# Kernel optimization log

Measured on AMD Instinct MI355X. Metric: run time of the kernel, lower is better.

## Reference

```python
import jax, jax.numpy as jnp
import numpy as np

B, S, D, H = 2, 4096, 128, 128
EPS = 1e-6
NEG_INF = -1e30


def _complex_linear(xr, xi, Wr, Wi, br, bi):
    # x: (B,S,D); W: (H,D); complex linear (Wr + i Wi)(xr + i xi) + (br + i bi) per layer math:
    # real_out = (xr Wr + br) - (xi Wi + bi); imag_out = (xi Wr + br) + (xr Wi + bi)
    out_r = xr @ Wr.T + br - (xi @ Wi.T + bi)
    out_i = xi @ Wr.T + br + (xr @ Wi.T + bi)
    return out_r, out_i


def setup_inputs() -> dict:
    key = jax.random.key(0)
    ks = jax.random.split(key, 24)
    scale = 1.0 / np.sqrt(D)
    def W(k):
        return jax.random.normal(k, (H, D), jnp.float32) * scale
    def b(k):
        return jax.random.normal(k, (H,), jnp.float32) * 0.01
    inp = {
        "Z_q": jax.random.normal(ks[0], (B, 2, S, D, 1), jnp.float32),
        "Z_k": jax.random.normal(ks[1], (B, 2, S, D, 1), jnp.float32),
        "Z_v": jax.random.normal(ks[2], (B, 2, S, D, 1), jnp.float32),
        "Wq_r": W(ks[3]), "Wq_i": W(ks[4]), "bq_r": b(ks[5]), "bq_i": b(ks[6]),
        "Wk_r": W(ks[7]), "Wk_i": W(ks[8]), "bk_r": b(ks[9]), "bk_i": b(ks[10]),
        "Wv_r": W(ks[11]), "Wv_i": W(ks[12]), "bv_r": b(ks[13]), "bv_i": b(ks[14]),
        "Wp_r": W(ks[15]), "Wp_i": W(ks[16]), "bp_r": b(ks[17]), "bp_i": b(ks[18]),
        "noise_floor": jnp.asarray(1.0, jnp.float32),
        "tau": jnp.asarray(0.0, jnp.float32),
    }
    return inp


def reference(Z_q, Z_k, Z_v,
              Wq_r, Wq_i, bq_r, bq_i,
              Wk_r, Wk_i, bk_r, bk_i,
              Wv_r, Wv_i, bv_r, bv_i,
              Wp_r, Wp_i, bp_r, bp_i,
              noise_floor, tau):
    # squeeze trailing singleton; split real/imag -> (B,S,D)
    zqr, zqi = Z_q[:, 0, :, :, 0], Z_q[:, 1, :, :, 0]
    zkr, zki = Z_k[:, 0, :, :, 0], Z_k[:, 1, :, :, 0]
    zvr, zvi = Z_v[:, 0, :, :, 0], Z_v[:, 1, :, :, 0]

    Qr, Qi = _complex_linear(zqr, zqi, Wq_r, Wq_i, bq_r, bq_i)
    Kr, Ki = _complex_linear(zkr, zki, Wk_r, Wk_i, bk_r, bk_i)
    Vr, Vi = _complex_linear(zvr, zvi, Wv_r, Wv_i, bv_r, bv_i)

    # InverseMahalanobis: R2[b,i,j] = sum_h |Q[b,i]-K[b,j]|^2
    q2 = jnp.sum(Qr * Qr + Qi * Qi, axis=-1)          # (B,S)
    k2 = jnp.sum(Kr * Kr + Ki * Ki, axis=-1)          # (B,S)
    re_qk = (jnp.einsum('bsh,bth->bst', Qr, Kr)
             + jnp.einsum('bsh,bth->bst', Qi, Ki))    # (B,S,S)
    R2 = q2[:, :, None] + k2[:, None, :] - 2.0 * re_qk

    attn_scores = -jax.nn.softplus(tau) * jnp.log(noise_floor ** 2 + R2 + EPS)
    mask = jnp.tril(jnp.ones((S, S), dtype=bool))[None]
    attn_scores = jnp.where(mask, attn_scores, NEG_INF)
    attn_weights = jax.nn.softmax(attn_scores / jnp.sqrt(jnp.float32(H)), axis=-1)

    # attn (real) times complex V
    est_r = jnp.einsum('bst,bth->bsh', attn_weights, Vr)
    est_i = jnp.einsum('bst,bth->bsh', attn_weights, Vi)

    out_r, out_i = _complex_linear(est_r, est_i, Wp_r, Wp_i, bp_r, bp_i)
    out = jnp.stack((out_r, out_i), axis=1)[..., None]  # (B,2,S,H,1)
    return out, attn_weights
```

## Files before the change

kernel.cpp:

```cpp
#include <hip/hip_runtime.h>

#define S_LEN 4096
#define NBATCH 2
#define OUT_ELEMS 2097152

typedef _Float16 f16;
typedef _Float16 f16x8 __attribute__((ext_vector_type(8)));
typedef _Float16 f16x4 __attribute__((ext_vector_type(4)));
typedef float f32x4 __attribute__((ext_vector_type(4)));

#define MT_OFF    0x000000
#define BIAS_OFF  0x080000
#define SC_OFF    0x081000
#define QH_OFF    0x100000
#define KH_OFF    0x500000
#define VH_OFF    0x900000
#define Q2_OFF    0xD00000
#define K2_OFF    0xD10000
#define L_OFF     0xD20000
#define VPT_OFF   0xE00000
#define PW_OFF    0x1600000
#define WS_NEED   0x5600000

#define MFMA16(A,B,C) __builtin_amdgcn_mfma_f32_16x16x32_f16(A,B,C,0,0,0)

__device__ __forceinline__ void async_cp16(f16* lds, const f16* g) {
  __builtin_amdgcn_global_load_lds(
      (const __attribute__((address_space(1))) void*)g,
      (__attribute__((address_space(3))) void*)lds, 16, 0, 0);
}


__device__ __forceinline__ void stage16(f16* lds, const f16* g, int stride, int tid) {
#pragma unroll
  for (int i = 0; i < 2; ++i) {
    int idx = i*256 + tid;
    int row = idx >> 2, c = idx & 3;
    int cs = c ^ ((row >> 1) & 3);
    async_cp16(lds + idx*8, g + (size_t)row*stride + cs*8);
  }
}

__device__ __forceinline__ void stage32(f16* lds, const float* g, int stride, int tid) {
#pragma unroll
  for (int i = 0; i < 4; ++i) {
    int idx = i*256 + tid;
    int row = idx >> 3, c = idx & 7;
    const float4* gp = (const float4*)(g + (size_t)row*stride + c*4);
    float4 v = *gp;
    f16x4 h; h[0]=(f16)v.x; h[1]=(f16)v.y; h[2]=(f16)v.z; h[3]=(f16)v.w;
    int cl = (((c >> 1) ^ ((row >> 1) & 3)) << 1) | (c & 1);
    *(f16x4*)(lds + row*32 + cl*4) = h;
  }
}

__device__ __forceinline__ void mfma_step(const f16* Asm, const f16* Bsm, int lane,
                                          int wm, int wn, f32x4 acc[4][4]) {
  f16x8 a[4], b[4];
  int rr = lane & 15;
  int sc = (lane >> 4) ^ ((rr >> 1) & 3);
#pragma unroll
  for (int i=0;i<4;i++) a[i] = *(const f16x8*)(Asm + (wm + i*16 + rr)*32 + (sc<<3));
#pragma unroll
  for (int j=0;j<4;j++) b[j] = *(const f16x8*)(Bsm + (wn + j*16 + rr)*32 + (sc<<3));
#pragma unroll
  for (int i=0;i<4;i++)
#pragma unroll
    for (int j=0;j<4;j++) acc[i][j] = MFMA16(a[i], b[j], acc[i][j]);
}

__global__ __launch_bounds__(256)
void k_build(const float* Wqr, const float* Wqi, const float* bqr, const float* bqi,
             const float* Wkr, const float* Wki, const float* bkr, const float* bki,
             const float* Wvr, const float* Wvi, const float* bvr, const float* bvi,
             const float* Wpr, const float* Wpi, const float* bpr, const float* bpi,
             f16* Mt, float* bias) {
  int mat = blockIdx.x;
  const float *Wr, *Wi, *br, *bi;
  if (mat == 0)      { Wr=Wqr; Wi=Wqi; br=bqr; bi=bqi; }
  else if (mat == 1) { Wr=Wkr; Wi=Wki; br=bkr; bi=bki; }
  else if (mat == 2) { Wr=Wvr; Wi=Wvi; br=bvr; bi=bvi; }
  else               { Wr=Wpr; Wi=Wpi; br=bpr; bi=bpi; }
  int idx = blockIdx.y*256 + threadIdx.x;
  int n = idx >> 8, k = idx & 255;
  int d = k & 127, h = n & 127;
  float w = (k < 128) ? ((n < 128) ? Wr[h*128+d] : Wi[h*128+d])
                      : ((n < 128) ? -Wi[h*128+d] : Wr[h*128+d]);
  Mt[mat*65536 + n*256 + k] = (f16)w;
  if (k == 0)
    bias[mat*256 + n] = (n < 128) ? (br[n] - bi[n]) : (br[n-128] + bi[n-128]);
}

__global__ __launch_bounds__(256)
void k_init(float* outp, float* attn, float* zreg, float* sc, const float* bias,
            const float* nf, const float* tau) {
  int bx = blockIdx.x, tid = threadIdx.x;
  float4 z = make_float4(0.f,0.f,0.f,0.f);
  if (bx < 992) {
    int b = bx >= 496; int r = bx - b*496;
    int tb = 1; while (r >= tb) { r -= tb; tb++; }
    int sb = r;
    float* base = attn + ((size_t)(b*S_LEN) + sb*128)*S_LEN + tb*128;
    int c4 = tid & 31;
#pragma unroll
    for (int it = 0; it < 16; ++it) {
      int row = it*8 + (tid >> 5);
      *(float4*)(base + (size_t)row*S_LEN + c4*4) = z;
    }
    return;
  }
  int idx = (bx - 992)*256 + tid;
  if (idx < 524288) {
    int h4 = idx & 31;
    int comp = (idx >> 17) & 1;
    ((float4*)outp)[idx] = *(const float4*)(bias + 3*256 + comp*128 + h4*4);
  } else {
    int j = idx - 524288;
    if (j < 12288) ((float4*)zreg)[j] = z;
  }
  if (idx == 0) {
    float t = tau[0];
    float c = __builtin_log2f(1.0f + __builtin_exp2f(t * 1.4426950408889634f))
              * 0.6931471805599453f;
    sc[0] = -c * 0.08838834764831845f;
    sc[1] = nf[0]*nf[0] + 1e-6f;
  }
}

__global__ __launch_bounds__(256)
void k_proj(const float* Zq, const float* Zk, const float* Zv,
            const f16* Mt, const float* bias,
            f16* Qh, f16* Kh, f16* Vh, float* q2, float* k2) {
  __shared__ f16 Asm[2][128*32];
  __shared__ f16 Bsm[2][128*32];
  __shared__ float bias_s[128];
  int tid = threadIdx.x;
  int mode = blockIdx.z;
  int m0 = blockIdx.x * 128, n0 = blockIdx.y * 128;
  const float* Z = (mode==0) ? Zq : (mode==1 ? Zk : Zv);
  const f16* Bt = Mt + mode*65536;
  if (tid < 128) bias_s[tid] = bias[mode*256 + n0 + tid];
  int b = m0 >> 12, s0 = m0 & 4095;
  int lane = tid & 63, w = tid >> 6;
  int wm = (w >> 1)*64, wn = (w & 1)*64;
  f32x4 acc[4][4] = {};
  {
    const float* Ag = Z + (((size_t)(b*2 + 0))*S_LEN + s0)*128 + 0;
    stage32(Asm[0], Ag, 128, tid);
    stage16(Bsm[0], Bt + n0*256 + 0, 256, tid);
  }
  __syncthreads();
  for (int kb = 0; kb < 8; ++kb) {
    int cur = kb & 1;
    if (kb < 7) {
      int k1 = (kb+1)*32;
      int part = k1 >> 7, d0 = k1 & 127;
      const float* Ag = Z + (((size_t)(b*2 + part))*S_LEN + s0)*128 + d0;
      stage32(Asm[cur^1], Ag, 128, tid);
      stage16(Bsm[cur^1], Bt + n0*256 + k1, 256, tid);
    }
    mfma_step(Asm[cur], Bsm[cur], lane, wm, wn, acc);
    __syncthreads();
  }
  int rr = (lane>>4)*4, cc = lane & 15;
  f16* O = (mode==0) ? Qh : (mode==1 ? Kh : Vh);
  float rs[4][4];
#pragma unroll
  for (int i=0;i<4;i++)
#pragma unroll
    for (int r=0;r<4;r++) rs[i][r]=0.f;
#pragma unroll
  for (int i=0;i<4;i++)
#pragma unroll
    for (int j=0;j<4;j++) {
      int cl = wn + j*16 + cc;
      int cg = n0 + cl;
      float bv = bias_s[cl];
#pragma unroll
      for (int r=0;r<4;r++) {
        int rg = m0 + wm + i*16 + rr + r;
        f16 hv = (f16)(acc[i][j][r] + bv);
        O[(size_t)rg*256 + cg] = hv;
        float fv = (float)hv;
        rs[i][r] += fv*fv;
      }
    }
  if (mode < 2) {
#pragma unroll
    for (int m=8;m>=1;m>>=1)
#pragma unroll
      for (int i=0;i<4;i++)
#pragma unroll
        for (int r=0;r<4;r++) rs[i][r] += __shfl_xor(rs[i][r], m, 64);
    if (cc == 0) {
      float* T = (mode==0) ? q2 : k2;
#pragma unroll
      for (int i=0;i<4;i++)
#pragma unroll
        for (int r=0;r<4;r++) {
          int rg = m0 + wm + i*16 + rr + r;
          atomicAdd(&T[rg], rs[i][r]);
        }
    }
  }
}

__global__ __launch_bounds__(256)
void k_vp(const f16* Vh, const f16* Mt, f16* VPt) {
  __shared__ f16 Asm[2][128*32];
  __shared__ f16 Bsm[2][128*32];
  int t0 = blockIdx.x*128, n0 = blockIdx.y*128, b = blockIdx.z;
  int tid = threadIdx.x;
  int lane = tid & 63, w = tid >> 6;
  int wm = (w>>1)*64, wn = (w&1)*64;
  const f16* Ag = Mt + 3*65536 + n0*256;
  const f16* Bg = Vh + ((size_t)(b*S_LEN) + t0)*256;
  f32x4 acc[4][4] = {};
  stage16(Asm[0], Ag, 256, tid);
  stage16(Bsm[0], Bg, 256, tid);
  __syncthreads();
  for (int kb=0;kb<8;kb++) {
    int cur = kb & 1;
    if (kb < 7) {
      stage16(Asm[cur^1], Ag + (kb+1)*32, 256, tid);
      stage16(Bsm[cur^1], Bg + (kb+1)*32, 256, tid);
    }
    mfma_step(Asm[cur], Bsm[cur], lane, wm, wn, acc);
    __syncthreads();
  }
  int rr = (lane>>4)*4, cc = lane & 15;
#pragma unroll
  for (int i=0;i<4;i++) {
    int n = n0 + wm + i*16 + rr;
#pragma unroll
    for (int j=0;j<4;j++) {
      int t = t0 + wn + j*16 + cc;
#pragma unroll
      for (int r=0;r<4;r++)
        VPt[(size_t)b*1048576 + (size_t)(n + r)*4096 + t] = (f16)acc[i][j][r];
    }
  }
}

__global__ __launch_bounds__(256)
void k_attn(const f16* Qh, const f16* Kh, const float* q2, const float* k2,
            const float* sc, float* lsum, f16* Pws) {
  __shared__ f16 smem[4*128*32];
  __shared__ float q2s[128], k2s[128];
  f16* Asm0 = smem;
  f16* Asm1 = smem + 4096;
  f16* Bsm0 = smem + 8192;
  f16* Bsm1 = smem + 12288;
  int x = blockIdx.x;
  int b = x >= 528; int r = x - b*528;
  int sb = 0; while (r > sb) { r -= sb + 1; sb++; }
  int tb = r;
  int s0 = sb*128, t0 = tb*128;
  int tid = threadIdx.x;
  if (tid < 128) {
    q2s[tid] = q2[b*S_LEN + s0 + tid];
    k2s[tid] = k2[b*S_LEN + t0 + tid];
  }
  float kc = sc[0], nf2 = sc[1];
  int lane = tid & 63, w = tid >> 6;
  int wm = (w >> 1)*64, wn = (w & 1)*64;
  const f16* Ag = Qh + ((size_t)(b*S_LEN) + s0)*256;
  const f16* Bg = Kh + ((size_t)(b*S_LEN) + t0)*256;
  f32x4 acc[4][4] = {};
  stage16(Asm0, Ag, 256, tid);
  stage16(Bsm0, Bg, 256, tid);
  __syncthreads();
  for (int kb=0;kb<8;kb++) {
    int cur = kb & 1;
    if (kb < 7) {
      stage16(cur ? Asm0 : Asm1, Ag + (kb+1)*32, 256, tid);
      stage16(cur ? Bsm0 : Bsm1, Bg + (kb+1)*32, 256, tid);
    }
    mfma_step(cur ? Asm1 : Asm0, cur ? Bsm1 : Bsm0, lane, wm, wn, acc);
    __syncthreads();
  }
  f16* Psm = smem;
  int rr = (lane>>4)*4, cc = lane & 15;
  bool diag = (tb == sb);
  float rs[4][4];
#pragma unroll
  for (int i=0;i<4;i++)
#pragma unroll
    for (int rg=0;rg<4;rg++) rs[i][rg]=0.f;
#pragma unroll
  for (int i=0;i<4;i++)
#pragma unroll
    for (int j=0;j<4;j++) {
      int cl = wn + j*16 + cc;
      float kv = k2s[cl];
#pragma unroll
      for (int rg=0;rg<4;rg++) {
        int rl = wm + i*16 + rr + rg;
        float xx = nf2 + q2s[rl] + kv - 2.0f*acc[i][j][rg];
        float P = __builtin_exp2f(kc * __builtin_log2f(__builtin_fmaxf(xx, 1e-6f)));
        if (diag && (t0+cl) > (s0+rl)) P = 0.f;
        Psm[rl*128 + cl] = (f16)P;
        rs[i][rg] += P;
      }
    }
  __syncthreads();
  f16* Pg = Pws + ((size_t)(b*S_LEN) + s0)*S_LEN + t0;
#pragma unroll
  for (int i2 = 0; i2 < 8; ++i2) {
    int idx = i2*256 + tid;
    int row = idx >> 4, c = idx & 15;
    *(f16x8*)(Pg + (size_t)row*S_LEN + c*8) = *(const f16x8*)(Psm + row*128 + c*8);
  }
#pragma unroll
  for (int m=8;m>=1;m>>=1)
#pragma unroll
    for (int i=0;i<4;i++)
#pragma unroll
      for (int rg=0;rg<4;rg++) rs[i][rg] += __shfl_xor(rs[i][rg], m, 64);
  if (cc == 0)
#pragma unroll
    for (int i=0;i<4;i++)
#pragma unroll
      for (int rg=0;rg<4;rg++) {
        int rl = wm + i*16 + rr + rg;
        atomicAdd(&lsum[b*S_LEN + s0 + rl], rs[i][rg]);
      }
}

__global__ __launch_bounds__(256)
void k_pv(const f16* Pws, const f16* VPt, const float* lsum, float* outp, float* attn) {
  __shared__ f16 Asm[2][128*32];
  __shared__ f16 Bsm[2][128*32];
  __shared__ float ls[128];
  int r = blockIdx.x;
  int nb = blockIdx.y, b = blockIdx.z;
  int sb = 0;
  while (r >= ((sb+4)>>2)) { r -= (sb+4)>>2; sb++; }
  int c = r;
  int s0 = sb*128, h0 = nb*128;
  int tid = threadIdx.x;
  bool wrb = (nb == 0);
  if (tid < 128) ls[tid] = 1.0f / lsum[b*S_LEN + s0 + tid];
  int lane = tid & 63, w = tid >> 6;
  int wm = (w>>1)*64, wn = (w&1)*64;
  int tb0 = c*4, tb1 = tb0 + 4; if (tb1 > sb+1) tb1 = sb+1;
  int nt = (tb1 - tb0) * 4;
  int base_t = tb0*128;
  const f16* Abase = Pws + ((size_t)(b*S_LEN) + s0)*S_LEN + base_t;
  const f16* Bbase = VPt + (size_t)b*1048576 + (size_t)h0*4096 + base_t;
  f32x4 acc[4][4] = {};
  int row2 = tid >> 1, half2 = tid & 1;
  int xs2 = (row2 >> 1) & 3;
  stage16(Asm[0], Abase, S_LEN, tid);
  stage16(Bsm[0], Bbase, 4096, tid);
  __syncthreads();
  for (int st = 0; st < nt; ++st) {
    int cur = st & 1;
    int t0 = base_t + st*32;
    if (st + 1 < nt) {
      stage16(Asm[cur^1], Abase + (st+1)*32, S_LEN, tid);
      stage16(Bsm[cur^1], Bbase + (st+1)*32, 4096, tid);
    }
    if (wrb) {
      float invl = ls[row2];
      const f16* Arow = Asm[cur] + row2*32;
      f16x8 v0 = *(const f16x8*)(Arow + (((2*half2  ) ^ xs2) << 3));
      f16x8 v1 = *(const f16x8*)(Arow + (((2*half2+1) ^ xs2) << 3));
      float4* dst = (float4*)(attn + ((size_t)(b*S_LEN) + s0 + row2)*S_LEN + t0 + half2*16);
      float4 o;
      o.x=(float)v0[0]*invl; o.y=(float)v0[1]*invl; o.z=(float)v0[2]*invl; o.w=(float)v0[3]*invl; dst[0]=o;
      o.x=(float)v0[4]*invl; o.y=(float)v0[5]*invl; o.z=(float)v0[6]*invl; o.w=(float)v0[7]*invl; dst[1]=o;
      o.x=(float)v1[0]*invl; o.y=(float)v1[1]*invl; o.z=(float)v1[2]*invl; o.w=(float)v1[3]*invl; dst[2]=o;
      o.x=(float)v1[4]*invl; o.y=(float)v1[5]*invl; o.z=(float)v1[6]*invl; o.w=(float)v1[7]*invl; dst[3]=o;
    }
    mfma_step(Asm[cur], Bsm[cur], lane, wm, wn, acc);
    __syncthreads();
  }
  int rr = (lane>>4)*4, cc = lane & 15;
#pragma unroll
  for (int i=0;i<4;i++)
#pragma unroll
    for (int j=0;j<4;j++) {
      int cg = h0 + wn + j*16 + cc;
      int comp = cg >> 7, h = cg & 127;
#pragma unroll
      for (int rg=0;rg<4;rg++) {
        int rl = wm + i*16 + rr + rg;
        float v = acc[i][j][rg] * ls[rl];
        atomicAdd(&outp[(((size_t)(b*2 + comp))*S_LEN + s0 + rl)*128 + h], v);
      }
    }
}

extern "C" void kernel_launch(void* const* d_in, const int* in_sizes, int n_in,
                              void* d_out, int out_size, void* d_ws, size_t ws_size,
                              hipStream_t stream) {
  (void)in_sizes; (void)n_in; (void)out_size;
  if (ws_size < (size_t)WS_NEED) return;
  const float* Zq = (const float*)d_in[0];
  const float* Zk = (const float*)d_in[1];
  const float* Zv = (const float*)d_in[2];
  char* ws = (char*)d_ws;
  f16*   Mt   = (f16*)(ws + MT_OFF);
  float* bias = (float*)(ws + BIAS_OFF);
  float* sc   = (float*)(ws + SC_OFF);
  f16*   Qh   = (f16*)(ws + QH_OFF);
  f16*   Kh   = (f16*)(ws + KH_OFF);
  f16*   Vh   = (f16*)(ws + VH_OFF);
  float* q2   = (float*)(ws + Q2_OFF);
  float* k2   = (float*)(ws + K2_OFF);
  float* lsum = (float*)(ws + L_OFF);
  f16*   VPt  = (f16*)(ws + VPT_OFF);
  f16*   Pws  = (f16*)(ws + PW_OFF);
  float* outp = (float*)d_out;
  float* attn = outp + OUT_ELEMS;

  k_build<<<dim3(4,256), 256, 0, stream>>>(
      (const float*)d_in[3],  (const float*)d_in[4],  (const float*)d_in[5],  (const float*)d_in[6],
      (const float*)d_in[7],  (const float*)d_in[8],  (const float*)d_in[9],  (const float*)d_in[10],
      (const float*)d_in[11], (const float*)d_in[12], (const float*)d_in[13], (const float*)d_in[14],
      (const float*)d_in[15], (const float*)d_in[16], (const float*)d_in[17], (const float*)d_in[18],
      Mt, bias);
  k_init<<<3088, 256, 0, stream>>>(outp, attn, q2, sc, bias,
                                   (const float*)d_in[19], (const float*)d_in[20]);
  k_proj<<<dim3(64,2,3), 256, 0, stream>>>(Zq, Zk, Zv, Mt, bias, Qh, Kh, Vh, q2, k2);
  k_vp<<<dim3(32,2,2), 256, 0, stream>>>(Vh, Mt, VPt);
  k_attn<<<1056, 256, 0, stream>>>(Qh, Kh, q2, k2, sc, lsum, Pws);
  k_pv<<<dim3(144,2,2), 256, 0, stream>>>(Pws, VPt, lsum, outp, attn);
}
```

Measured before the change: 310.1 us.

## Fold output projection into V projection and widen PV blocks to full head dim

Precomputes the product of the V and output projection matrices (and the combined bias) in a small kernel. V is then projected straight into the transposed VPt layout inside k_proj, which removes the separate k_vp GEMM and the Vh buffer. k_proj now stages its outputs through shared memory so the global stores are coalesced. k_pv uses 512 threads covering all 256 output columns per block, so each P tile is read and the attention weights are written once instead of across two column blocks. The cost is an extra fp16 rounding of the fused weight matrix and higher register and LDS use per PV block.

Measured after the change: 303.2 us. 2.2% less time.

```diff
diff --git a/kernel.cpp b/kernel.cpp
--- a/kernel.cpp
+++ b/kernel.cpp
@@ -1,7 +1,6 @@
 #include <hip/hip_runtime.h>
 
 #define S_LEN 4096
-#define NBATCH 2
 #define OUT_ELEMS 2097152
 
 typedef _Float16 f16;
@@ -12,9 +11,10 @@
 #define MT_OFF    0x000000
 #define BIAS_OFF  0x080000
 #define SC_OFF    0x081000
+#define BVP_OFF   0x082000
+#define W2_OFF    0x090000
 #define QH_OFF    0x100000
 #define KH_OFF    0x500000
-#define VH_OFF    0x900000
 #define Q2_OFF    0xD00000
 #define K2_OFF    0xD10000
 #define L_OFF     0xD20000
@@ -92,6 +92,22 @@
 }
 
 __global__ __launch_bounds__(256)
+void k_build2(const f16* Mt, const float* bias, f16* W2t, float* bvp) {
+  int n = blockIdx.x, k = threadIdx.x;
+  const f16* Mtv = Mt + 2*65536;
+  const f16* Mtp = Mt + 3*65536;
+  float acc = 0.f;
+  for (int j = 0; j < 256; ++j)
+    acc += (float)Mtv[j*256 + k] * (float)Mtp[n*256 + j];
+  W2t[n*256 + k] = (f16)acc;
+  if (k == 0) {
+    float a = 0.f;
+    for (int j = 0; j < 256; ++j) a += bias[2*256 + j] * (float)Mtp[n*256 + j];
+    bvp[n] = a;
+  }
+}
+
+__global__ __launch_bounds__(256)
 void k_init(float* outp, float* attn, float* zreg, float* sc, const float* bias,
             const float* nf, const float* tau) {
   int bx = blockIdx.x, tid = threadIdx.x;
@@ -129,25 +145,28 @@
 
 __global__ __launch_bounds__(256)
 void k_proj(const float* Zq, const float* Zk, const float* Zv,
-            const f16* Mt, const float* bias,
-            f16* Qh, f16* Kh, f16* Vh, float* q2, float* k2) {
-  __shared__ f16 Asm[2][128*32];
-  __shared__ f16 Bsm[2][128*32];
+            const f16* Mt, const f16* W2t, const float* bias, const float* bvp,
+            f16* Qh, f16* Kh, f16* VPt, float* q2, float* k2) {
+  __shared__ f16 smem[17408];
   __shared__ float bias_s[128];
+  f16* A0 = smem;
+  f16* A1 = smem + 4096;
+  f16* B0 = smem + 8192;
+  f16* B1 = smem + 12288;
   int tid = threadIdx.x;
   int mode = blockIdx.z;
   int m0 = blockIdx.x * 128, n0 = blockIdx.y * 128;
   const float* Z = (mode==0) ? Zq : (mode==1 ? Zk : Zv);
-  const f16* Bt = Mt + mode*65536;
-  if (tid < 128) bias_s[tid] = bias[mode*256 + n0 + tid];
+  const f16* Bt = (mode==2) ? W2t : (Mt + mode*65536);
+  if (tid < 128) bias_s[tid] = (mode==2) ? bvp[n0 + tid] : bias[mode*256 + n0 + tid];
   int b = m0 >> 12, s0 = m0 & 4095;
   int lane = tid & 63, w = tid >> 6;
   int wm = (w >> 1)*64, wn = (w & 1)*64;
   f32x4 acc[4][4] = {};
   {
     const float* Ag = Z + (((size_t)(b*2 + 0))*S_LEN + s0)*128 + 0;
-    stage32(Asm[0], Ag, 128, tid);
-    stage16(Bsm[0], Bt + n0*256 + 0, 256, tid);
+    stage32(A0, Ag, 128, tid);
+    stage16(B0, Bt + n0*256 + 0, 256, tid);
   }
   __syncthreads();
   for (int kb = 0; kb < 8; ++kb) {
@@ -156,36 +175,58 @@
       int k1 = (kb+1)*32;
       int part = k1 >> 7, d0 = k1 & 127;
       const float* Ag = Z + (((size_t)(b*2 + part))*S_LEN + s0)*128 + d0;
-      stage32(Asm[cur^1], Ag, 128, tid);
-      stage16(Bsm[cur^1], Bt + n0*256 + k1, 256, tid);
-    }
-    mfma_step(Asm[cur], Bsm[cur], lane, wm, wn, acc);
+      stage32(cur ? A0 : A1, Ag, 128, tid);
+      stage16(cur ? B0 : B1, Bt + n0*256 + k1, 256, tid);
+    }
+    mfma_step(cur ? A1 : A0, cur ? B1 : B0, lane, wm, wn, acc);
     __syncthreads();
   }
-  int rr = (lane>>4)*4, cc = lane & 15;
-  f16* O = (mode==0) ? Qh : (mode==1 ? Kh : Vh);
+  int rr2 = (lane>>4)*4, cc = lane & 15;
+  f16* Osm = smem;
   float rs[4][4];
 #pragma unroll
   for (int i=0;i<4;i++)
 #pragma unroll
     for (int r=0;r<4;r++) rs[i][r]=0.f;
-#pragma unroll
-  for (int i=0;i<4;i++)
-#pragma unroll
-    for (int j=0;j<4;j++) {
-      int cl = wn + j*16 + cc;
-      int cg = n0 + cl;
-      float bv = bias_s[cl];
-#pragma unroll
-      for (int r=0;r<4;r++) {
-        int rg = m0 + wm + i*16 + rr + r;
-        f16 hv = (f16)(acc[i][j][r] + bv);
-        O[(size_t)rg*256 + cg] = hv;
-        float fv = (float)hv;
-        rs[i][r] += fv*fv;
-      }
-    }
   if (mode < 2) {
+#pragma unroll
+    for (int i=0;i<4;i++)
+#pragma unroll
+      for (int j=0;j<4;j++) {
+        int cl = wn + j*16 + cc;
+        float bv = bias_s[cl];
+#pragma unroll
+        for (int r=0;r<4;r++) {
+          int rl = wm + i*16 + rr2 + r;
+          f16 hv = (f16)(acc[i][j][r] + bv);
+          Osm[rl*136 + cl] = hv;
+          float fv = (float)hv;
+          rs[i][r] += fv*fv;
+        }
+      }
+  } else {
+#pragma unroll
+    for (int i=0;i<4;i++)
+#pragma unroll
+      for (int j=0;j<4;j++) {
+        int cl = wn + j*16 + cc;
+        float bv = bias_s[cl];
+#pragma unroll
+        for (int r=0;r<4;r++) {
+          int rl = wm + i*16 + rr2 + r;
+          Osm[cl*136 + rl] = (f16)(acc[i][j][r] + bv);
+        }
+      }
+  }
+  __syncthreads();
+  if (mode < 2) {
+    f16* O = (mode==0) ? Qh : Kh;
+#pragma unroll
+    for (int i2 = 0; i2 < 8; ++i2) {
+      int idx = i2*256 + tid;
+      int row = idx >> 4, c = idx & 15;
+      *(f16x8*)(O + (size_t)(m0+row)*256 + n0 + c*8) = *(const f16x8*)(Osm + row*136 + c*8);
+    }
 #pragma unroll
     for (int m=8;m>=1;m>>=1)
 #pragma unroll
@@ -198,46 +239,17 @@
       for (int i=0;i<4;i++)
 #pragma unroll
         for (int r=0;r<4;r++) {
-          int rg = m0 + wm + i*16 + rr + r;
+          int rg = m0 + wm + i*16 + rr2 + r;
           atomicAdd(&T[rg], rs[i][r]);
         }
     }
-  }
-}
-
-__global__ __launch_bounds__(256)
-void k_vp(const f16* Vh, const f16* Mt, f16* VPt) {
-  __shared__ f16 Asm[2][128*32];
-  __shared__ f16 Bsm[2][128*32];
-  int t0 = blockIdx.x*128, n0 = blockIdx.y*128, b = blockIdx.z;
-  int tid = threadIdx.x;
-  int lane = tid & 63, w = tid >> 6;
-  int wm = (w>>1)*64, wn = (w&1)*64;
-  const f16* Ag = Mt + 3*65536 + n0*256;
-  const f16* Bg = Vh + ((size_t)(b*S_LEN) + t0)*256;
-  f32x4 acc[4][4] = {};
-  stage16(Asm[0], Ag, 256, tid);
-  stage16(Bsm[0], Bg, 256, tid);
-  __syncthreads();
-  for (int kb=0;kb<8;kb++) {
-    int cur = kb & 1;
-    if (kb < 7) {
-      stage16(Asm[cur^1], Ag + (kb+1)*32, 256, tid);
-      stage16(Bsm[cur^1], Bg + (kb+1)*32, 256, tid);
-    }
-    mfma_step(Asm[cur], Bsm[cur], lane, wm, wn, acc);
-    __syncthreads();
-  }
-  int rr = (lane>>4)*4, cc = lane & 15;
-#pragma unroll
-  for (int i=0;i<4;i++) {
-    int n = n0 + wm + i*16 + rr;
-#pragma unroll
-    for (int j=0;j<4;j++) {
-      int t = t0 + wn + j*16 + cc;
-#pragma unroll
-      for (int r=0;r<4;r++)
-        VPt[(size_t)b*1048576 + (size_t)(n + r)*4096 + t] = (f16)acc[i][j][r];
+  } else {
+#pragma unroll
+    for (int i2 = 0; i2 < 8; ++i2) {
+      int idx = i2*256 + tid;
+      int row = idx >> 4, c = idx & 15;
+      *(f16x8*)(VPt + (size_t)b*1048576 + (size_t)(n0+row)*4096 + s0 + c*8)
+          = *(const f16x8*)(Osm + row*136 + c*8);
     }
   }
 }
@@ -327,65 +339,76 @@
       }
 }
 
-__global__ __launch_bounds__(256)
+__global__ __launch_bounds__(512)
 void k_pv(const f16* Pws, const f16* VPt, const float* lsum, float* outp, float* attn) {
   __shared__ f16 Asm[2][128*32];
-  __shared__ f16 Bsm[2][128*32];
+  __shared__ f16 Bsm[2][256*32];
   __shared__ float ls[128];
-  int r = blockIdx.x;
-  int nb = blockIdx.y, b = blockIdx.z;
+  int r = blockIdx.x, b = blockIdx.y;
   int sb = 0;
   while (r >= ((sb+4)>>2)) { r -= (sb+4)>>2; sb++; }
   int c = r;
-  int s0 = sb*128, h0 = nb*128;
+  int s0 = sb*128;
   int tid = threadIdx.x;
-  bool wrb = (nb == 0);
   if (tid < 128) ls[tid] = 1.0f / lsum[b*S_LEN + s0 + tid];
   int lane = tid & 63, w = tid >> 6;
-  int wm = (w>>1)*64, wn = (w&1)*64;
+  int wm = (w>>2)*64, wn = (w&3)*64;
   int tb0 = c*4, tb1 = tb0 + 4; if (tb1 > sb+1) tb1 = sb+1;
   int nt = (tb1 - tb0) * 4;
   int base_t = tb0*128;
   const f16* Abase = Pws + ((size_t)(b*S_LEN) + s0)*S_LEN + base_t;
-  const f16* Bbase = VPt + (size_t)b*1048576 + (size_t)h0*4096 + base_t;
+  const f16* Bbase = VPt + (size_t)b*1048576 + base_t;
   f32x4 acc[4][4] = {};
-  int row2 = tid >> 1, half2 = tid & 1;
-  int xs2 = (row2 >> 1) & 3;
-  stage16(Asm[0], Abase, S_LEN, tid);
-  stage16(Bsm[0], Bbase, 4096, tid);
+  {
+    int row = tid >> 2, cc0 = tid & 3, cs = cc0 ^ ((row >> 1) & 3);
+    async_cp16(Asm[0] + tid*8, Abase + (size_t)row*S_LEN + cs*8);
+  }
+#pragma unroll
+  for (int i=0;i<2;i++) {
+    int idx = i*512 + tid, row = idx >> 2, cc0 = idx & 3, cs = cc0 ^ ((row >> 1) & 3);
+    async_cp16(Bsm[0] + idx*8, Bbase + (size_t)row*4096 + cs*8);
+  }
   __syncthreads();
   for (int st = 0; st < nt; ++st) {
     int cur = st & 1;
-    int t0 = base_t + st*32;
+    int tcur = base_t + st*32;
     if (st + 1 < nt) {
-      stage16(Asm[cur^1], Abase + (st+1)*32, S_LEN, tid);
-      stage16(Bsm[cur^1], Bbase + (st+1)*32, 4096, tid);
-    }
-    if (wrb) {
-      float invl = ls[row2];
-      const f16* Arow = Asm[cur] + row2*32;
-      f16x8 v0 = *(const f16x8*)(Arow + (((2*half2  ) ^ xs2) << 3));
-      f16x8 v1 = *(const f16x8*)(Arow + (((2*half2+1) ^ xs2) << 3));
-      float4* dst = (float4*)(attn + ((size_t)(b*S_LEN) + s0 + row2)*S_LEN + t0 + half2*16);
+      const f16* Ag = Abase + (st+1)*32;
+      const f16* Bg = Bbase + (st+1)*32;
+      {
+        int row = tid >> 2, cc0 = tid & 3, cs = cc0 ^ ((row >> 1) & 3);
+        async_cp16(Asm[cur^1] + tid*8, Ag + (size_t)row*S_LEN + cs*8);
+      }
+#pragma unroll
+      for (int i=0;i<2;i++) {
+        int idx = i*512 + tid, row = idx >> 2, cc0 = idx & 3, cs = cc0 ^ ((row >> 1) & 3);
+        async_cp16(Bsm[cur^1] + idx*8, Bg + (size_t)row*4096 + cs*8);
+      }
+    }
+#pragma unroll
+    for (int i2=0;i2<2;i2++) {
+      int idx = i2*512 + tid, row = idx >> 3, c4 = idx & 7;
+      int cs = (c4 >> 1) ^ ((row >> 1) & 3);
+      f16x4 v = *(const f16x4*)(Asm[cur] + row*32 + cs*8 + (c4 & 1)*4);
+      float invl = ls[row];
       float4 o;
-      o.x=(float)v0[0]*invl; o.y=(float)v0[1]*invl; o.z=(float)v0[2]*invl; o.w=(float)v0[3]*invl; dst[0]=o;
-      o.x=(float)v0[4]*invl; o.y=(float)v0[5]*invl; o.z=(float)v0[6]*invl; o.w=(float)v0[7]*invl; dst[1]=o;
-      o.x=(float)v1[0]*invl; o.y=(float)v1[1]*invl; o.z=(float)v1[2]*invl; o.w=(float)v1[3]*invl; dst[2]=o;
-      o.x=(float)v1[4]*invl; o.y=(float)v1[5]*invl; o.z=(float)v1[6]*invl; o.w=(float)v1[7]*invl; dst[3]=o;
+      o.x=(float)v[0]*invl; o.y=(float)v[1]*invl;
+      o.z=(float)v[2]*invl; o.w=(float)v[3]*invl;
+      *(float4*)(attn + ((size_t)(b*S_LEN) + s0 + row)*S_LEN + tcur + c4*4) = o;
     }
     mfma_step(Asm[cur], Bsm[cur], lane, wm, wn, acc);
     __syncthreads();
   }
-  int rr = (lane>>4)*4, cc = lane & 15;
+  int rr2 = (lane>>4)*4, cc = lane & 15;
 #pragma unroll
   for (int i=0;i<4;i++)
 #pragma unroll
     for (int j=0;j<4;j++) {
-      int cg = h0 + wn + j*16 + cc;
+      int cg = wn + j*16 + cc;
       int comp = cg >> 7, h = cg & 127;
 #pragma unroll
       for (int rg=0;rg<4;rg++) {
-        int rl = wm + i*16 + rr + rg;
+        int rl = wm + i*16 + rr2 + rg;
         float v = acc[i][j][rg] * ls[rl];
         atomicAdd(&outp[(((size_t)(b*2 + comp))*S_LEN + s0 + rl)*128 + h], v);
       }
@@ -404,9 +427,10 @@
   f16*   Mt   = (f16*)(ws + MT_OFF);
   float* bias = (float*)(ws + BIAS_OFF);
   float* sc   = (float*)(ws + SC_OFF);
+  float* bvp  = (float*)(ws + BVP_OFF);
+  f16*   W2t  = (f16*)(ws + W2_OFF);
   f16*   Qh   = (f16*)(ws + QH_OFF);
   f16*   Kh   = (f16*)(ws + KH_OFF);
-  f16*   Vh   = (f16*)(ws + VH_OFF);
   float* q2   = (float*)(ws + Q2_OFF);
   float* k2   = (float*)(ws + K2_OFF);
   float* lsum = (float*)(ws + L_OFF);
@@ -421,10 +445,11 @@
       (const float*)d_in[11], (const float*)d_in[12], (const float*)d_in[13], (const float*)d_in[14],
       (const float*)d_in[15], (const float*)d_in[16], (const float*)d_in[17], (const float*)d_in[18],
       Mt, bias);
+  k_build2<<<256, 256, 0, stream>>>(Mt, bias, W2t, bvp);
   k_init<<<3088, 256, 0, stream>>>(outp, attn, q2, sc, bias,
                                    (const float*)d_in[19], (const float*)d_in[20]);
-  k_proj<<<dim3(64,2,3), 256, 0, stream>>>(Zq, Zk, Zv, Mt, bias, Qh, Kh, Vh, q2, k2);
-  k_vp<<<dim3(32,2,2), 256, 0, stream>>>(Vh, Mt, VPt);
+  k_proj<<<dim3(64,2,3), 256, 0, stream>>>(Zq, Zk, Zv, Mt, W2t, bias, bvp,
+                                           Qh, Kh, VPt, q2, k2);
   k_attn<<<1056, 256, 0, stream>>>(Qh, Kh, q2, k2, sc, lsum, Pws);
-  k_pv<<<dim3(144,2,2), 256, 0, stream>>>(Pws, VPt, lsum, outp, attn);
-}
+  k_pv<<<dim3(144,2), 512, 0, stream>>>(Pws, VPt, lsum, outp, attn);
+}
```
